# Optimization experiments

Measured on AMD Instinct MI355X. Metric: run time of the kernel, lower is better.

The kernel has to match this reference:

```python
import jax, jax.numpy as jnp
import numpy as np

D_MODEL = 1024
N_HEADS = 16
DK = D_MODEL // N_HEADS


def setup_inputs() -> dict:
    key = jax.random.key(0)
    ks = jax.random.split(key, 5)
    scale = 1.0 / np.sqrt(D_MODEL)
    x = jax.random.normal(ks[0], (2, 2048, D_MODEL), dtype=jnp.float32)
    Wq = jax.random.normal(ks[1], (D_MODEL, D_MODEL), dtype=jnp.float32) * scale
    Wk = jax.random.normal(ks[2], (D_MODEL, D_MODEL), dtype=jnp.float32) * scale
    Wv = jax.random.normal(ks[3], (D_MODEL, D_MODEL), dtype=jnp.float32) * scale
    Wo = jax.random.normal(ks[4], (D_MODEL, D_MODEL), dtype=jnp.float32) * scale
    return {"x": x, "Wq": Wq, "Wk": Wk, "Wv": Wv, "Wo": Wo}


def reference(x, Wq, Wk, Wv, Wo):
    B, S, D = x.shape
    # Projections (nn.Linear applies x @ W.T; weights here are stored as [out, in])
    q = (x @ Wq.T).reshape(B, S, N_HEADS, DK).transpose(0, 2, 1, 3)  # [B,H,S,dk]
    k = (x @ Wk.T).reshape(B, S, N_HEADS, DK).transpose(0, 2, 1, 3)
    v = (x @ Wv.T).reshape(B, S, N_HEADS, DK).transpose(0, 2, 1, 3)
    scores = jnp.einsum("bhqd,bhkd->bhqk", q, k) / jnp.sqrt(jnp.asarray(DK, x.dtype))
    # Note: original's mask branch is a non-in-place masked_fill (no-op); softmax is unmasked.
    attn = jax.nn.softmax(scores, axis=-1)
    out = jnp.einsum("bhqk,bhkd->bhqd", attn, v)  # [B,H,S,dk]
    out = out.transpose(0, 2, 1, 3).reshape(B, S, D)
    return out @ Wo.T
```

## Files before the change

### kernel.cpp

```cpp
#include <hip/hip_runtime.h>
#include <hip/hip_bf16.h>


typedef __attribute__((ext_vector_type(8))) short bf16x8;
typedef __attribute__((ext_vector_type(4))) float f32x4;

#define SEQ     2048

__device__ __forceinline__ unsigned short f2bf(float f) {
    unsigned u = __builtin_bit_cast(unsigned, f);
    u = (u + 0x7FFFu + ((u >> 16) & 1u)) >> 16;
    return (unsigned short)u;
}

__device__ __forceinline__ float bf2f(unsigned short v) {
    return __builtin_bit_cast(float, ((unsigned)v) << 16);
}

__device__ __forceinline__ unsigned pack_bf2(float lo, float hi) {
    return (unsigned)f2bf(lo) | ((unsigned)f2bf(hi) << 16);
}

__device__ __forceinline__ float fexp2(float x) {
    return exp2f(x);
}

__device__ __forceinline__ void gload16(const void* g, void* l) {
    __builtin_amdgcn_global_load_lds(
        (const __attribute__((address_space(1))) unsigned int*)g,
        (__attribute__((address_space(3))) unsigned int*)l, 16, 0, 0);
}

__global__ __launch_bounds__(256) void cast_all(
    const float* __restrict__ x,
    const float* __restrict__ wq, const float* __restrict__ wk,
    const float* __restrict__ wv, const float* __restrict__ wo,
    short* __restrict__ xb,
    short* __restrict__ wqb, short* __restrict__ wkb,
    short* __restrict__ wvb, short* __restrict__ wob)
{
    int bid = blockIdx.x;
    const float* src; short* dst; long base;
    if (bid < 2048) { src = x; dst = xb; base = (long)bid * 2048; }
    else {
        int k = (bid - 2048) >> 9;
        int r = (bid - 2048) & 511;
        base = (long)r * 2048;
        src = (k == 0) ? wq : (k == 1) ? wk : (k == 2) ? wv : wo;
        dst = (k == 0) ? wqb : (k == 1) ? wkb : (k == 2) ? wvb : wob;
    }
    long off = base + (long)threadIdx.x * 8;
    float4 a = *(const float4*)&src[off];
    float4 b = *(const float4*)&src[off + 4];
    union { unsigned short us[8]; uint4 u; } pk;
    pk.us[0] = f2bf(a.x); pk.us[1] = f2bf(a.y); pk.us[2] = f2bf(a.z); pk.us[3] = f2bf(a.w);
    pk.us[4] = f2bf(b.x); pk.us[5] = f2bf(b.y); pk.us[6] = f2bf(b.z); pk.us[7] = f2bf(b.w);
    *(uint4*)&dst[off] = pk.u;
}

__global__ __launch_bounds__(256) void gemm_qkv(
    const short* __restrict__ A,
    const short* __restrict__ W0, const short* __restrict__ W1, const short* __restrict__ W2,
    short* __restrict__ D0, short* __restrict__ D1, short* __restrict__ D2)
{
    __shared__ short At[128 * 32];
    __shared__ short Bt[128 * 32];
    const int tid = threadIdx.x;
    const int w = tid >> 6, l = tid & 63, lg = l >> 4, ln = l & 15;
    const int wr = w >> 1, wc = w & 1;
    const int reg = blockIdx.x >> 3;
    const short* W = (reg == 0) ? W0 : (reg == 1) ? W1 : W2;
    short* Dst     = (reg == 0) ? D0 : (reg == 1) ? D1 : D2;
    const float sc = (reg == 0) ? 0.18033688011112042f : 1.0f;
    const long col0 = (long)(blockIdx.x & 7) * 128;
    const long row0 = (long)blockIdx.y * 128;
    const char* Ab = (const char*)A;
    const char* Wb = (const char*)W;

    f32x4 acc[4][4] = {};

    for (int k0 = 0; k0 < 1024; k0 += 32) {
        __syncthreads();
#pragma unroll
        for (int c = 0; c < 2; ++c) {
            int lin = (c * 4 + w) * 1024 + l * 16;
            int r = lin >> 6, cb = lin & 63;
            gload16(Ab + (size_t)(row0 + r) * 2048 + (size_t)k0 * 2 + cb,
                    (char*)At + (c * 4 + w) * 1024);
            gload16(Wb + (size_t)(col0 + r) * 2048 + (size_t)k0 * 2 + cb,
                    (char*)Bt + (c * 4 + w) * 1024);
        }
        __syncthreads();

        bf16x8 af[4], bfr[4];
#pragma unroll
        for (int i = 0; i < 4; ++i)
            af[i] = *(const bf16x8*)&At[(wr * 64 + i * 16 + ln) * 32 + lg * 8];
#pragma unroll
        for (int j = 0; j < 4; ++j)
            bfr[j] = *(const bf16x8*)&Bt[(wc * 64 + j * 16 + ln) * 32 + lg * 8];
#pragma unroll
        for (int i = 0; i < 4; ++i)
#pragma unroll
            for (int j = 0; j < 4; ++j)
                acc[i][j] = __builtin_amdgcn_mfma_f32_16x16x32_bf16(af[i], bfr[j], acc[i][j], 0, 0, 0);
    }

#pragma unroll
    for (int i = 0; i < 4; ++i)
#pragma unroll
        for (int j = 0; j < 4; ++j)
#pragma unroll
            for (int rr = 0; rr < 4; ++rr) {
                long grow = row0 + wr * 64 + i * 16 + lg * 4 + rr;
                long gcol = col0 + wc * 64 + j * 16 + ln;
                Dst[grow * 1024 + gcol] = (short)f2bf(acc[i][j][rr] * sc);
            }
}

__global__ __launch_bounds__(256) void gemm_bt_f32(
    const short* __restrict__ A, const short* __restrict__ W, float* __restrict__ Cout)
{
    __shared__ short At[128 * 32];
    __shared__ short Bt[128 * 32];
    const int tid = threadIdx.x;
    const int w = tid >> 6, l = tid & 63, lg = l >> 4, ln = l & 15;
    const int wr = w >> 1, wc = w & 1;
    const long row0 = (long)blockIdx.y * 128;
    const long col0 = (long)blockIdx.x * 128;
    const char* Ab = (const char*)A;
    const char* Wb = (const char*)W;

    f32x4 acc[4][4] = {};

    for (int k0 = 0; k0 < 1024; k0 += 32) {
        __syncthreads();
#pragma unroll
        for (int c = 0; c < 2; ++c) {
            int lin = (c * 4 + w) * 1024 + l * 16;
            int r = lin >> 6, cb = lin & 63;
            gload16(Ab + (size_t)(row0 + r) * 2048 + (size_t)k0 * 2 + cb,
                    (char*)At + (c * 4 + w) * 1024);
            gload16(Wb + (size_t)(col0 + r) * 2048 + (size_t)k0 * 2 + cb,
                    (char*)Bt + (c * 4 + w) * 1024);
        }
        __syncthreads();

        bf16x8 af[4], bfr[4];
#pragma unroll
        for (int i = 0; i < 4; ++i)
            af[i] = *(const bf16x8*)&At[(wr * 64 + i * 16 + ln) * 32 + lg * 8];
#pragma unroll
        for (int j = 0; j < 4; ++j)
            bfr[j] = *(const bf16x8*)&Bt[(wc * 64 + j * 16 + ln) * 32 + lg * 8];
#pragma unroll
        for (int i = 0; i < 4; ++i)
#pragma unroll
            for (int j = 0; j < 4; ++j)
                acc[i][j] = __builtin_amdgcn_mfma_f32_16x16x32_bf16(af[i], bfr[j], acc[i][j], 0, 0, 0);
    }

#pragma unroll
    for (int i = 0; i < 4; ++i)
#pragma unroll
        for (int j = 0; j < 4; ++j)
#pragma unroll
            for (int rr = 0; rr < 4; ++rr) {
                long grow = row0 + wr * 64 + i * 16 + lg * 4 + rr;
                long gcol = col0 + wc * 64 + j * 16 + ln;
                Cout[grow * 1024 + gcol] = acc[i][j][rr];
            }
}

__global__ __launch_bounds__(256) void transpose_bf16(
    const short* __restrict__ V, short* __restrict__ VT)
{
    __shared__ short t[64][66];
    const int tid = threadIdx.x;
    const int r = tid >> 2, c4 = (tid & 3) * 16;
    const long m0 = (long)blockIdx.y * 64;
    const long n0 = (long)blockIdx.x * 64;
#pragma unroll
    for (int j = 0; j < 2; ++j) {
        bf16x8 v = *(const bf16x8*)&V[(m0 + r) * 1024 + n0 + c4 + j * 8];
#pragma unroll
        for (int e = 0; e < 8; ++e) t[c4 + j * 8 + e][r] = v[e];
    }
    __syncthreads();
#pragma unroll
    for (int j = 0; j < 2; ++j) {
        bf16x8 v;
#pragma unroll
        for (int e = 0; e < 8; ++e) v[e] = t[r][c4 + j * 8 + e];
        *(bf16x8*)&VT[(n0 + r) * 4096 + m0 + c4 + j * 8] = v;
    }
}

__global__ __launch_bounds__(256, 6) void attn_part(
    const short* __restrict__ Q, const short* __restrict__ K,
    const short* __restrict__ VT,
    short* __restrict__ OP0, short* __restrict__ OP1,
    float2* __restrict__ ML0, float2* __restrict__ ML1)
{
    __shared__ short Kt[64 * 64];
    __shared__ short Vt[64 * 64];
    __shared__ short Pt[4 * 1024];

    const int tid = threadIdx.x;
    const int w = tid >> 6, l = tid & 63, lg = l >> 4, ln = l & 15;
    const int bh = blockIdx.y, b = bh >> 4, h = bh & 15;
    const int qt = blockIdx.x >> 1, half = blockIdx.x & 1;
    const long qrow0 = (long)b * SEQ + (long)qt * 64;

    short*  __restrict__ OPh = half ? OP1 : OP0;
    float2* __restrict__ MLh = half ? ML1 : ML0;

    bf16x8 qf[2];
#pragma unroll
    for (int kk = 0; kk < 2; ++kk)
        qf[kk] = *(const bf16x8*)&Q[(qrow0 + w * 16 + ln) * 1024 + h * 64 + kk * 32 + lg * 8];

    f32x4 o[4] = {};
    float m_run = -1e30f, l_run = 0.f;

    const char* Kb  = (const char*)K;
    const char* VTb = (const char*)VT;

    char*       Pw = (char*)Pt + w * 2048 + l * 8;
    const char* Pr = (char*)Pt + w * 2048 + (lg >> 1) * 512 + (lg & 1) * 256 + ln * 8;

    for (int t = half * 16; t < half * 16 + 16; ++t) {
        __syncthreads();
#pragma unroll
        for (int c = 0; c < 2; ++c) {
            int lin = (c * 4 + w) * 1024 + l * 16;
            int r = lin >> 7;
            int cb = (lin & 127) ^ ((r & 7) << 4);
            gload16(Kb + (size_t)(b * SEQ + t * 64 + r) * 2048 + h * 128 + cb,
                    (char*)Kt + (c * 4 + w) * 1024);
            gload16(VTb + (size_t)(h * 64 + r) * 8192 + (size_t)(b * SEQ + t * 64) * 2 + cb,
                    (char*)Vt + (c * 4 + w) * 1024);
        }
        __syncthreads();

        f32x4 s[4] = {};
#pragma unroll
        for (int nb = 0; nb < 4; ++nb) {
            int row = nb * 16 + ln;
#pragma unroll
            for (int kk = 0; kk < 2; ++kk) {
                int cb = (kk * 64 + lg * 16) ^ ((row & 7) << 4);
                bf16x8 kf = *(const bf16x8*)((const char*)Kt + row * 128 + cb);
                s[nb] = __builtin_amdgcn_mfma_f32_16x16x32_bf16(kf, qf[kk], s[nb], 0, 0, 0);
            }
        }

        float mx = s[0][0];
#pragma unroll
        for (int nb = 0; nb < 4; ++nb)
#pragma unroll
            for (int i = 0; i < 4; ++i) mx = fmaxf(mx, s[nb][i]);
        mx = fmaxf(mx, __shfl_xor(mx, 16, 64));
        mx = fmaxf(mx, __shfl_xor(mx, 32, 64));

        if (__any(mx > m_run + 8.0f)) {
            float mn = fmaxf(m_run, mx);
            float fac = fexp2(m_run - mn);
            m_run = mn;
            l_run *= fac;
            float facr[4];
#pragma unroll
            for (int i = 0; i < 4; ++i)
                facr[i] = __shfl(fac, 16 * lg + lg * 4 + i, 64);
#pragma unroll
            for (int nb = 0; nb < 4; ++nb)
#pragma unroll
                for (int i = 0; i < 4; ++i) o[nb][i] *= facr[i];
        }

        float p[4][4];
        float sum = 0.f;
#pragma unroll
        for (int nb = 0; nb < 4; ++nb)
#pragma unroll
            for (int i = 0; i < 4; ++i) {
                float pv = fexp2(s[nb][i] - m_run);
                p[nb][i] = pv;
                sum += pv;
            }
        sum += __shfl_xor(sum, 16, 64);
        sum += __shfl_xor(sum, 32, 64);
        l_run += sum;

#pragma unroll
        for (int nb = 0; nb < 4; ++nb) {
            uint2 pw = { pack_bf2(p[nb][0], p[nb][1]), pack_bf2(p[nb][2], p[nb][3]) };
            *(uint2*)(Pw + nb * 512) = pw;
        }

        bf16x8 pa[2];
#pragma unroll
        for (int kk = 0; kk < 2; ++kk) {
            uint2 d0 = *(const uint2*)(Pr + kk * 1024);
            uint2 d1 = *(const uint2*)(Pr + kk * 1024 + 128);
            uint4 u4 = { d0.x, d0.y, d1.x, d1.y };
            pa[kk] = __builtin_bit_cast(bf16x8, u4);
        }
#pragma unroll
        for (int nb = 0; nb < 4; ++nb) {
            int row = nb * 16 + ln;
#pragma unroll
            for (int kk = 0; kk < 2; ++kk) {
                int cb = (kk * 64 + lg * 16) ^ ((row & 7) << 4);
                bf16x8 vf = *(const bf16x8*)((const char*)Vt + row * 128 + cb);
                o[nb] = __builtin_amdgcn_mfma_f32_16x16x32_bf16(pa[kk], vf, o[nb], 0, 0, 0);
            }
        }
    }

    const long Rbase = (long)bh * SEQ + qt * 64 + w * 16;
#pragma unroll
    for (int nb = 0; nb < 4; ++nb)
#pragma unroll
        for (int i = 0; i < 4; ++i) {
            long R = Rbase + lg * 4 + i;
            OPh[R * 64 + nb * 16 + ln] = (short)f2bf(o[nb][i]);
        }
    if (lg == 0)
        MLh[Rbase + ln] = float2{ m_run, l_run };
}

__global__ __launch_bounds__(256) void attn_merge(
    const short* __restrict__ O0, const short* __restrict__ O1,
    const float2* __restrict__ ML0, const float2* __restrict__ ML1,
    short* __restrict__ Ab)
{
    int gid = blockIdx.x * 256 + threadIdx.x;
    int R = gid >> 3, d0 = (gid & 7) * 8;
    float2 a = ML0[R];
    float2 c = ML1[R];
    float M = fmaxf(a.x, c.x);
    float w0 = fexp2(a.x - M), w1 = fexp2(c.x - M);
    float rden = 1.0f / (w0 * a.y + w1 * c.y);
    bf16x8 v0 = *(const bf16x8*)&O0[(long)R * 64 + d0];
    bf16x8 v1 = *(const bf16x8*)&O1[(long)R * 64 + d0];
    int bh = R >> 11, s = R & 2047, b = bh >> 4, h = bh & 15;
    union { unsigned short us[8]; uint4 u; } pk;
#pragma unroll
    for (int e = 0; e < 8; ++e) {
        float f0 = bf2f((unsigned short)v0[e]);
        float f1 = bf2f((unsigned short)v1[e]);
        pk.us[e] = f2bf((w0 * f0 + w1 * f1) * rden);
    }
    *(uint4*)&Ab[((long)(b * 2048 + s)) * 1024 + h * 64 + d0] = pk.u;
}

extern "C" void kernel_launch(void* const* d_in, const int* in_sizes, int n_in,
                              void* d_out, int out_size, void* d_ws, size_t ws_size,
                              hipStream_t stream)
{
    const float* x  = (const float*)d_in[0];
    const float* wq = (const float*)d_in[1];
    const float* wk = (const float*)d_in[2];
    const float* wv = (const float*)d_in[3];
    const float* wo = (const float*)d_in[4];
    float* out = (float*)d_out;
    char* ws = (char*)d_ws;

    const size_t MB = 1024 * 1024;
    short* Xb  = (short*)(ws);
    short* Wqb = (short*)(ws + 8  * MB);
    short* Wkb = (short*)(ws + 10 * MB);
    short* Wvb = (short*)(ws + 12 * MB);
    short* Wob = (short*)(ws + 14 * MB);
    short* Qb  = (short*)(ws + 16 * MB);
    short* Kb  = (short*)(ws + 24 * MB);
    short* Vb  = (short*)(ws + 32 * MB);
    short* VTb = (short*)(ws + 40 * MB);
    short* Ab  = (short*)(ws + 48 * MB);
    short*  OP0 = (short*)(ws);
    float2* ML0 = (float2*)(ws + 8 * MB);
    float2* ML1 = (float2*)(ws + 8 * MB + 512 * 1024);
    short*  OP1 = (short*)(ws + 32 * MB);

    cast_all<<<4096, 256, 0, stream>>>(x, wq, wk, wv, wo, Xb, Wqb, Wkb, Wvb, Wob);

    gemm_qkv<<<dim3(24, 32), 256, 0, stream>>>(Xb, Wqb, Wkb, Wvb, Qb, Kb, Vb);

    transpose_bf16<<<dim3(16, 64), 256, 0, stream>>>(Vb, VTb);

    attn_part<<<dim3(64, 32), 256, 0, stream>>>(Qb, Kb, VTb, OP0, OP1, ML0, ML1);

    attn_merge<<<2048, 256, 0, stream>>>(OP0, OP1, ML0, ML1, Ab);

    gemm_bt_f32<<<dim3(8, 32), 256, 0, stream>>>(Ab, Wob, out);
}
```

Baseline: 222.5 us.

## Double-buffer LDS tiles in GEMMs and attention with smaller KV tiles

Both projection GEMMs now use two LDS buffers, so the next K-slice is fetched while MFMAs run on the current one, with one barrier per iteration instead of two. The attention kernel gets the same double buffering, and its KV tile shrinks from 64 to 32 keys so the doubled buffers still fit in less LDS. Its occupancy hint is raised from 6 to 8 blocks per CU. The cost is more loop iterations and barriers in attention, less work per barrier, and extra register pressure from the higher occupancy target.

Result: no change. 224.6 us (+0.9%).

```diff
diff --git a/kernel.cpp b/kernel.cpp
--- a/kernel.cpp
+++ b/kernel.cpp
@@ -63,8 +63,8 @@
     const short* __restrict__ W0, const short* __restrict__ W1, const short* __restrict__ W2,
     short* __restrict__ D0, short* __restrict__ D1, short* __restrict__ D2)
 {
-    __shared__ short At[128 * 32];
-    __shared__ short Bt[128 * 32];
+    __shared__ short At[2][128 * 32];
+    __shared__ short Bt[2][128 * 32];
     const int tid = threadIdx.x;
     const int w = tid >> 6, l = tid & 63, lg = l >> 4, ln = l & 15;
     const int wr = w >> 1, wc = w & 1;
@@ -79,31 +79,39 @@
 
     f32x4 acc[4][4] = {};
 
-    for (int k0 = 0; k0 < 1024; k0 += 32) {
-        __syncthreads();
+    auto STAGE = [&](int buf, int k0) {
 #pragma unroll
         for (int c = 0; c < 2; ++c) {
             int lin = (c * 4 + w) * 1024 + l * 16;
             int r = lin >> 6, cb = lin & 63;
             gload16(Ab + (size_t)(row0 + r) * 2048 + (size_t)k0 * 2 + cb,
-                    (char*)At + (c * 4 + w) * 1024);
+                    (char*)At[buf] + (c * 4 + w) * 1024);
             gload16(Wb + (size_t)(col0 + r) * 2048 + (size_t)k0 * 2 + cb,
-                    (char*)Bt + (c * 4 + w) * 1024);
-        }
-        __syncthreads();
+                    (char*)Bt[buf] + (c * 4 + w) * 1024);
+        }
+    };
+
+    STAGE(0, 0);
+    __syncthreads();
+
+    for (int k0 = 0; k0 < 1024; k0 += 32) {
+        const int buf = (k0 >> 5) & 1;
+        if (k0 + 32 < 1024) STAGE(buf ^ 1, k0 + 32);
 
         bf16x8 af[4], bfr[4];
 #pragma unroll
         for (int i = 0; i < 4; ++i)
-            af[i] = *(const bf16x8*)&At[(wr * 64 + i * 16 + ln) * 32 + lg * 8];
+            af[i] = *(const bf16x8*)&At[buf][(wr * 64 + i * 16 + ln) * 32 + lg * 8];
 #pragma unroll
         for (int j = 0; j < 4; ++j)
-            bfr[j] = *(const bf16x8*)&Bt[(wc * 64 + j * 16 + ln) * 32 + lg * 8];
+            bfr[j] = *(const bf16x8*)&Bt[buf][(wc * 64 + j * 16 + ln) * 32 + lg * 8];
 #pragma unroll
         for (int i = 0; i < 4; ++i)
 #pragma unroll
             for (int j = 0; j < 4; ++j)
                 acc[i][j] = __builtin_amdgcn_mfma_f32_16x16x32_bf16(af[i], bfr[j], acc[i][j], 0, 0, 0);
+
+        __syncthreads();
     }
 
 #pragma unroll
@@ -121,8 +129,8 @@
 __global__ __launch_bounds__(256) void gemm_bt_f32(
     const short* __restrict__ A, const short* __restrict__ W, float* __restrict__ Cout)
 {
-    __shared__ short At[128 * 32];
-    __shared__ short Bt[128 * 32];
+    __shared__ short At[2][128 * 32];
+    __shared__ short Bt[2][128 * 32];
     const int tid = threadIdx.x;
     const int w = tid >> 6, l = tid & 63, lg = l >> 4, ln = l & 15;
     const int wr = w >> 1, wc = w & 1;
@@ -133,31 +141,39 @@
 
     f32x4 acc[4][4] = {};
 
-    for (int k0 = 0; k0 < 1024; k0 += 32) {
-        __syncthreads();
+    auto STAGE = [&](int buf, int k0) {
 #pragma unroll
         for (int c = 0; c < 2; ++c) {
             int lin = (c * 4 + w) * 1024 + l * 16;
             int r = lin >> 6, cb = lin & 63;
             gload16(Ab + (size_t)(row0 + r) * 2048 + (size_t)k0 * 2 + cb,
-                    (char*)At + (c * 4 + w) * 1024);
+                    (char*)At[buf] + (c * 4 + w) * 1024);
             gload16(Wb + (size_t)(col0 + r) * 2048 + (size_t)k0 * 2 + cb,
-                    (char*)Bt + (c * 4 + w) * 1024);
-        }
-        __syncthreads();
+                    (char*)Bt[buf] + (c * 4 + w) * 1024);
+        }
+    };
+
+    STAGE(0, 0);
+    __syncthreads();
+
+    for (int k0 = 0; k0 < 1024; k0 += 32) {
+        const int buf = (k0 >> 5) & 1;
+        if (k0 + 32 < 1024) STAGE(buf ^ 1, k0 + 32);
 
         bf16x8 af[4], bfr[4];
 #pragma unroll
         for (int i = 0; i < 4; ++i)
-            af[i] = *(const bf16x8*)&At[(wr * 64 + i * 16 + ln) * 32 + lg * 8];
+            af[i] = *(const bf16x8*)&At[buf][(wr * 64 + i * 16 + ln) * 32 + lg * 8];
 #pragma unroll
         for (int j = 0; j < 4; ++j)
-            bfr[j] = *(const bf16x8*)&Bt[(wc * 64 + j * 16 + ln) * 32 + lg * 8];
+            bfr[j] = *(const bf16x8*)&Bt[buf][(wc * 64 + j * 16 + ln) * 32 + lg * 8];
 #pragma unroll
         for (int i = 0; i < 4; ++i)
 #pragma unroll
             for (int j = 0; j < 4; ++j)
                 acc[i][j] = __builtin_amdgcn_mfma_f32_16x16x32_bf16(af[i], bfr[j], acc[i][j], 0, 0, 0);
+
+        __syncthreads();
     }
 
 #pragma unroll
@@ -196,15 +212,15 @@
     }
 }
 
-__global__ __launch_bounds__(256, 6) void attn_part(
+__global__ __launch_bounds__(256, 8) void attn_part(
     const short* __restrict__ Q, const short* __restrict__ K,
     const short* __restrict__ VT,
     short* __restrict__ OP0, short* __restrict__ OP1,
     float2* __restrict__ ML0, float2* __restrict__ ML1)
 {
-    __shared__ short Kt[64 * 64];
-    __shared__ short Vt[64 * 64];
-    __shared__ short Pt[4 * 1024];
+    __shared__ short Kt[2][32 * 64];
+    __shared__ short Vt[2][64 * 32];
+    __shared__ short Pt[4 * 512];
 
     const int tid = threadIdx.x;
     const int w = tid >> 6, l = tid & 63, lg = l >> 4, ln = l & 15;
@@ -226,38 +242,47 @@
     const char* Kb  = (const char*)K;
     const char* VTb = (const char*)VT;
 
-    char*       Pw = (char*)Pt + w * 2048 + l * 8;
-    const char* Pr = (char*)Pt + w * 2048 + (lg >> 1) * 512 + (lg & 1) * 256 + ln * 8;
-
-    for (int t = half * 16; t < half * 16 + 16; ++t) {
-        __syncthreads();
-#pragma unroll
-        for (int c = 0; c < 2; ++c) {
-            int lin = (c * 4 + w) * 1024 + l * 16;
-            int r = lin >> 7;
-            int cb = (lin & 127) ^ ((r & 7) << 4);
-            gload16(Kb + (size_t)(b * SEQ + t * 64 + r) * 2048 + h * 128 + cb,
-                    (char*)Kt + (c * 4 + w) * 1024);
-            gload16(VTb + (size_t)(h * 64 + r) * 8192 + (size_t)(b * SEQ + t * 64) * 2 + cb,
-                    (char*)Vt + (c * 4 + w) * 1024);
-        }
-        __syncthreads();
-
-        f32x4 s[4] = {};
-#pragma unroll
-        for (int nb = 0; nb < 4; ++nb) {
+    const int lin = w * 1024 + l * 16;
+    const int rK = lin >> 7, cbK = (lin & 127) ^ ((rK & 7) << 4);
+    const int rV = lin >> 6, cbV = (lin & 63) ^ ((rV & 3) << 4);
+    const size_t vrow = (size_t)(h * 64 + rV) * 8192 + (size_t)b * SEQ * 2 + cbV;
+
+    char*       Pw = (char*)Pt + w * 1024 + l * 8;
+    const char* Pr = (char*)Pt + w * 1024 + (lg >> 1) * 512 + (lg & 1) * 256 + ln * 8;
+
+    const int t0 = half * 32;
+
+    gload16(Kb + (size_t)(b * SEQ + t0 * 32 + rK) * 2048 + h * 128 + cbK,
+            (char*)Kt[0] + w * 1024);
+    gload16(VTb + vrow + (size_t)t0 * 64,
+            (char*)Vt[0] + w * 1024);
+    __syncthreads();
+
+    for (int tt = 0; tt < 32; ++tt) {
+        const int buf = tt & 1;
+        if (tt + 1 < 32) {
+            const int t = t0 + tt + 1;
+            gload16(Kb + (size_t)(b * SEQ + t * 32 + rK) * 2048 + h * 128 + cbK,
+                    (char*)Kt[buf ^ 1] + w * 1024);
+            gload16(VTb + vrow + (size_t)t * 64,
+                    (char*)Vt[buf ^ 1] + w * 1024);
+        }
+
+        f32x4 s[2] = {};
+#pragma unroll
+        for (int nb = 0; nb < 2; ++nb) {
             int row = nb * 16 + ln;
 #pragma unroll
             for (int kk = 0; kk < 2; ++kk) {
                 int cb = (kk * 64 + lg * 16) ^ ((row & 7) << 4);
-                bf16x8 kf = *(const bf16x8*)((const char*)Kt + row * 128 + cb);
+                bf16x8 kf = *(const bf16x8*)((const char*)Kt[buf] + row * 128 + cb);
                 s[nb] = __builtin_amdgcn_mfma_f32_16x16x32_bf16(kf, qf[kk], s[nb], 0, 0, 0);
             }
         }
 
         float mx = s[0][0];
 #pragma unroll
-        for (int nb = 0; nb < 4; ++nb)
+        for (int nb = 0; nb < 2; ++nb)
 #pragma unroll
             for (int i = 0; i < 4; ++i) mx = fmaxf(mx, s[nb][i]);
         mx = fmaxf(mx, __shfl_xor(mx, 16, 64));
@@ -278,10 +303,10 @@
                 for (int i = 0; i < 4; ++i) o[nb][i] *= facr[i];
         }
 
-        float p[4][4];
+        float p[2][4];
         float sum = 0.f;
 #pragma unroll
-        for (int nb = 0; nb < 4; ++nb)
+        for (int nb = 0; nb < 2; ++nb)
 #pragma unroll
             for (int i = 0; i < 4; ++i) {
                 float pv = fexp2(s[nb][i] - m_run);
@@ -293,29 +318,24 @@
         l_run += sum;
 
 #pragma unroll
-        for (int nb = 0; nb < 4; ++nb) {
+        for (int nb = 0; nb < 2; ++nb) {
             uint2 pw = { pack_bf2(p[nb][0], p[nb][1]), pack_bf2(p[nb][2], p[nb][3]) };
             *(uint2*)(Pw + nb * 512) = pw;
         }
 
-        bf16x8 pa[2];
-#pragma unroll
-        for (int kk = 0; kk < 2; ++kk) {
-            uint2 d0 = *(const uint2*)(Pr + kk * 1024);
-            uint2 d1 = *(const uint2*)(Pr + kk * 1024 + 128);
-            uint4 u4 = { d0.x, d0.y, d1.x, d1.y };
-            pa[kk] = __builtin_bit_cast(bf16x8, u4);
-        }
+        uint2 d0 = *(const uint2*)(Pr);
+        uint2 d1 = *(const uint2*)(Pr + 128);
+        uint4 u4 = { d0.x, d0.y, d1.x, d1.y };
+        bf16x8 pa = __builtin_bit_cast(bf16x8, u4);
 #pragma unroll
         for (int nb = 0; nb < 4; ++nb) {
             int row = nb * 16 + ln;
-#pragma unroll
-            for (int kk = 0; kk < 2; ++kk) {
-                int cb = (kk * 64 + lg * 16) ^ ((row & 7) << 4);
-                bf16x8 vf = *(const bf16x8*)((const char*)Vt + row * 128 + cb);
-                o[nb] = __builtin_amdgcn_mfma_f32_16x16x32_bf16(pa[kk], vf, o[nb], 0, 0, 0);
-            }
-        }
+            int cb = (lg * 16) ^ ((row & 3) << 4);
+            bf16x8 vf = *(const bf16x8*)((const char*)Vt[buf] + row * 64 + cb);
+            o[nb] = __builtin_amdgcn_mfma_f32_16x16x32_bf16(pa, vf, o[nb], 0, 0, 0);
+        }
+
+        __syncthreads();
     }
 
     const long Rbase = (long)bh * SEQ + qt * 64 + w * 16;
```
